# Performance work log

Hardware: AMD Instinct MI355X
Metric: run time of the kernel (lower is better)

Reference implementation:

```python
import jax, jax.numpy as jnp
import numpy as np

N_NODES = 100000
N_EDGES = 1600000
NFEAT = 256
NHID = 128
NCLASS = 2
NEG_SLOPE = 0.2


def setup_inputs() -> dict:
    key = jax.random.key(0)
    ks = jax.random.split(key, 8)
    x = jax.random.normal(ks[0], (N_NODES, NFEAT), dtype=jnp.float32)
    edge_index = jax.random.randint(ks[1], (2, N_EDGES), 0, N_NODES, dtype=jnp.int64)
    # GATConv params (heads=1): lin weight (no bias), att_src, att_dst, bias
    W = jax.random.normal(ks[2], (NFEAT, NHID), dtype=jnp.float32) * (1.0 / np.sqrt(NFEAT))
    att_src = jax.random.normal(ks[3], (NHID,), dtype=jnp.float32) * (1.0 / np.sqrt(NHID))
    att_dst = jax.random.normal(ks[4], (NHID,), dtype=jnp.float32) * (1.0 / np.sqrt(NHID))
    bias_gat = jnp.zeros((NHID,), dtype=jnp.float32)
    fc_w = jax.random.normal(ks[5], (NCLASS, NHID), dtype=jnp.float32) * (1.0 / np.sqrt(NHID))
    fc_b = jnp.zeros((NCLASS,), dtype=jnp.float32)
    return {"x": x, "edge_index": edge_index, "W": W, "att_src": att_src,
            "att_dst": att_dst, "bias_gat": bias_gat, "fc_w": fc_w, "fc_b": fc_b}


def reference(x, edge_index, W, att_src, att_dst, bias_gat, fc_w, fc_b):
    N = x.shape[0]
    # add self loops (PyG GATConv default)
    loops = jnp.broadcast_to(jnp.arange(N, dtype=edge_index.dtype)[None, :], (2, N))
    ei = jnp.concatenate([edge_index, loops], axis=1)  # [2, E+N]
    src, dst = ei[0], ei[1]

    h = x @ W                                 # [N, NHID]
    a_src = h @ att_src                       # [N]
    a_dst = h @ att_dst                       # [N]

    e = jax.nn.leaky_relu(a_src[src] + a_dst[dst], NEG_SLOPE)  # [E+N]
    # segment softmax over destination nodes (every node has a self loop)
    m = jax.ops.segment_max(e, dst, num_segments=N)
    ex = jnp.exp(e - m[dst])
    s = jax.ops.segment_sum(ex, dst, num_segments=N)
    alpha = ex / (s[dst] + 1e-16)             # [E+N]

    msg = h[src] * alpha[:, None]             # [E+N, NHID]
    out = jax.ops.segment_sum(msg, dst, num_segments=N) + bias_gat  # [N, NHID]

    logits = out @ fc_w.T + fc_b              # [N, NCLASS]
    return jax.nn.log_softmax(logits, axis=1)
```

## Files before the change

kernel.cpp:

```cpp
#include <hip/hip_runtime.h>
#include <hip/hip_bf16.h>
#include <stdint.h>

#define N_NODES 100000
#define N_EDGES 1600000
#define NFEAT   256
#define NHID    128
#define NEG_SLOPE 0.2f

#define NB_B       3125
#define SLAB       1024
#define BIN_BLOCKS 512

typedef __attribute__((ext_vector_type(8))) short short8;
typedef __attribute__((ext_vector_type(4))) float f32x4;

__device__ __forceinline__ int clamp_node(int v) {
    unsigned u = (unsigned)v;
    return (u < (unsigned)N_NODES) ? (int)u : 0;
}

__device__ __forceinline__ unsigned short f2bf(float f) {
    unsigned u = __float_as_uint(f);
    return (unsigned short)((u + 0x7fffu + ((u >> 16) & 1u)) >> 16);
}
__device__ __forceinline__ unsigned pkbf(float a, float b) {
    __hip_bfloat162 t = __float22bfloat162_rn(make_float2(a, b));
    return *reinterpret_cast<unsigned*>(&t);
}
__device__ __forceinline__ float bflo(unsigned p) { return __uint_as_float(p << 16); }
__device__ __forceinline__ float bfhi(unsigned p) { return __uint_as_float(p & 0xffff0000u); }

__global__ __launch_bounds__(256) void k_conv(
    const float* __restrict__ W, unsigned short* __restrict__ Wt)
{
    int id = blockIdx.x * 256 + threadIdx.x;
    int n = id >> 8, k = id & 255;
    Wt[id] = f2bf(W[k * NHID + n]);
}

#define LDS_STRIDE 40
__global__ __launch_bounds__(256) void k_gemm_mfma(
    const float* __restrict__ x,
    const unsigned short* __restrict__ Wt,
    const float* __restrict__ atts,
    const float* __restrict__ attd,
    unsigned short* __restrict__ hb,
    float* __restrict__ asrc,
    float* __restrict__ adst)
{
    __shared__ unsigned short As[64 * LDS_STRIDE];
    __shared__ float satt[64][2];

    const int tid  = threadIdx.x;
    const int wave = tid >> 6;
    const int lane = tid & 63;
    const int wm = wave >> 1, wn = wave & 1;
    const int lr = lane & 15, q = lane >> 4;
    const int blockM = blockIdx.x * 64;

    const int ar = tid >> 2;
    const int aq = tid & 3;

    if (tid < 64) { satt[tid][0] = 0.f; satt[tid][1] = 0.f; }

    f32x4 acc[2][4];
#pragma unroll
    for (int a = 0; a < 2; ++a)
#pragma unroll
        for (int b = 0; b < 4; ++b) acc[a][b] = 0.f;

    const int growA = min(blockM + ar, N_NODES - 1);
    const float* xrow = x + (size_t)growA * NFEAT + aq * 8;

    const unsigned short* bbase[4];
#pragma unroll
    for (int nt = 0; nt < 4; ++nt)
        bbase[nt] = Wt + (size_t)(wn * 64 + nt * 16 + lr) * NFEAT + q * 8;

    float4 va0, va1;
    {
        const float4* xp = (const float4*)xrow;
        va0 = xp[0]; va1 = xp[1];
    }
    short8 bcur[4], bnxt[4];
#pragma unroll
    for (int nt = 0; nt < 4; ++nt)
        bcur[nt] = *(const short8*)(bbase[nt]);

#pragma unroll
    for (int kt = 0; kt < 8; ++kt) {
        __syncthreads();
        uint4 pa = make_uint4(pkbf(va0.x, va0.y), pkbf(va0.z, va0.w),
                              pkbf(va1.x, va1.y), pkbf(va1.z, va1.w));
        *(uint4*)&As[ar * LDS_STRIDE + aq * 8] = pa;
        __syncthreads();

        if (kt < 7) {
            const float4* xp = (const float4*)(xrow + (kt + 1) * 32);
            va0 = xp[0]; va1 = xp[1];
#pragma unroll
            for (int nt = 0; nt < 4; ++nt)
                bnxt[nt] = *(const short8*)(bbase[nt] + (kt + 1) * 32);
        }

        short8 af[2];
#pragma unroll
        for (int mt = 0; mt < 2; ++mt)
            af[mt] = *(const short8*)&As[(wm * 32 + mt * 16 + lr) * LDS_STRIDE + q * 8];

#pragma unroll
        for (int mt = 0; mt < 2; ++mt)
#pragma unroll
            for (int nt = 0; nt < 4; ++nt)
                acc[mt][nt] = __builtin_amdgcn_mfma_f32_16x16x32_bf16(
                    af[mt], bcur[nt], acc[mt][nt], 0, 0, 0);

#pragma unroll
        for (int nt = 0; nt < 4; ++nt) bcur[nt] = bnxt[nt];
    }

    float attsv[4], attdv[4];
#pragma unroll
    for (int nt = 0; nt < 4; ++nt) {
        attsv[nt] = atts[wn * 64 + nt * 16 + lr];
        attdv[nt] = attd[wn * 64 + nt * 16 + lr];
    }
#pragma unroll
    for (int mt = 0; mt < 2; ++mt) {
#pragma unroll
        for (int reg = 0; reg < 4; ++reg) {
            float s = 0.f, d = 0.f;
#pragma unroll
            for (int nt = 0; nt < 4; ++nt) {
                float v = acc[mt][nt][reg];
                s += v * attsv[nt];
                d += v * attdv[nt];
            }
#pragma unroll
            for (int mask = 8; mask > 0; mask >>= 1) {
                s += __shfl_xor(s, mask);
                d += __shfl_xor(d, mask);
            }
            if (lr == 0) {
                int lrow = wm * 32 + mt * 16 + q * 4 + reg;
                atomicAdd(&satt[lrow][0], s);
                atomicAdd(&satt[lrow][1], d);
            }
        }
    }

#pragma unroll
    for (int mt = 0; mt < 2; ++mt) {
#pragma unroll
        for (int reg = 0; reg < 4; ++reg) {
            int grow = blockM + wm * 32 + mt * 16 + q * 4 + reg;
            if (grow < N_NODES) {
                unsigned short* hp = hb + (size_t)grow * NHID + wn * 64 + lr;
#pragma unroll
                for (int nt = 0; nt < 4; ++nt)
                    hp[nt * 16] = f2bf(acc[mt][nt][reg]);
            }
        }
    }

    __syncthreads();
    if (tid < 64) {
        int g = blockM + tid;
        if (g < N_NODES) {
            asrc[g] = satt[tid][0];
            adst[g] = satt[tid][1];
        }
    }
}

__global__ __launch_bounds__(256) void k_bin(
    const int* __restrict__ ei, int* __restrict__ gcur,
    unsigned* __restrict__ staged)
{
    __shared__ int hist[NB_B];
    __shared__ int base[NB_B];
    const int t = threadIdx.x;
    const int per = (N_EDGES + BIN_BLOCKS - 1) / BIN_BLOCKS;
    const int e0 = blockIdx.x * per;
    const int e1 = min(e0 + per, N_EDGES);

    for (int i = t; i < NB_B; i += 256) hist[i] = 0;
    __syncthreads();
    for (int e = e0 + t; e < e1; e += 256)
        atomicAdd(&hist[clamp_node(ei[N_EDGES + e]) >> 5], 1);
    __syncthreads();
    for (int i = t; i < NB_B; i += 256) {
        int c = hist[i];
        base[i] = c ? atomicAdd(&gcur[i], c) : 0;
        hist[i] = 0;
    }
    __syncthreads();
    for (int e = e0 + t; e < e1; e += 256) {
        int d = clamp_node(ei[N_EDGES + e]);
        int s = clamp_node(ei[e]);
        int b = d >> 5;
        int pos = base[b] + atomicAdd(&hist[b], 1);
        if (pos < SLAB)
            staged[(size_t)b * SLAB + pos] = (unsigned)s | ((unsigned)(d & 31) << 17);
    }
}

__global__ __launch_bounds__(256) void k_sort_agg(
    const unsigned* __restrict__ staged, const int* __restrict__ gcur,
    const float* __restrict__ asrc, const float* __restrict__ adst,
    const unsigned short* __restrict__ hb,
    const float* __restrict__ bias, const float* __restrict__ fcw,
    const float* __restrict__ fcb, float* __restrict__ out)
{
    __shared__ float2 buf[SLAB];
    __shared__ int hist[32], scanv[32], cntv[32];
    __shared__ float asrc_s[32], adst_s[32];

    const int b = blockIdx.x;
    const int t = threadIdx.x;
    const int eb = b * SLAB;
    const int n = min(gcur[b], SLAB);
    const int nodeStart = b * 32;

    if (t < 32) {
        hist[t] = 0;
        adst_s[t] = adst[nodeStart + t];
        asrc_s[t] = asrc[nodeStart + t];
    }
    __syncthreads();

    for (int j = t; j < n; j += 256)
        atomicAdd(&hist[(staged[eb + j] >> 17) & 31], 1);
    __syncthreads();

    if (t < 32) {
        int v = hist[t];
        int sc = v;
#pragma unroll
        for (int off = 1; off < 32; off <<= 1) {
            int u = __shfl_up(sc, off);
            if (t >= off) sc += u;
        }
        scanv[t] = sc - v;
        cntv[t] = v;
        hist[t] = 0;
    }
    __syncthreads();

    for (int j = t; j < n; j += 256) {
        unsigned pk = staged[eb + j];
        int s  = pk & 0x1FFFF;
        int dl = (pk >> 17) & 31;
        float a = asrc[s] + adst_s[dl];
        a = (a > 0.f) ? a : NEG_SLOPE * a;
        float ew = __expf(fminf(a, 60.f));
        int pos = scanv[dl] + atomicAdd(&hist[dl], 1);
        buf[pos] = make_float2(__int_as_float(s), ew);
    }
    __syncthreads();

    const int wave = t >> 6;
    const int lane = t & 63;
    const unsigned* hrows = (const unsigned*)hb;

    const float b0 = bias[2 * lane], b1 = bias[2 * lane + 1];
    const float w00 = fcw[2 * lane], w01 = fcw[2 * lane + 1];
    const float w10 = fcw[NHID + 2 * lane], w11 = fcw[NHID + 2 * lane + 1];
    const float fb0 = fcb[0], fb1 = fcb[1];

    for (int ln = wave * 8; ln < wave * 8 + 8; ++ln) {
        int i = nodeStart + ln;

        float e0 = asrc_s[ln] + adst_s[ln];
        e0 = (e0 > 0.f) ? e0 : NEG_SLOPE * e0;
        float w = __expf(fminf(e0, 60.f));
        unsigned pself = hrows[(unsigned)i * 64u + lane];
        float accx = w * bflo(pself), accy = w * bfhi(pself), ssum = w;

        const int jb = scanv[ln];
        const int nn = cntv[ln];
        int j = 0;
        for (; j + 8 <= nn; j += 8) {
            float2 m[8];
            unsigned p[8];
#pragma unroll
            for (int u = 0; u < 8; ++u) m[u] = buf[jb + j + u];
#pragma unroll
            for (int u = 0; u < 8; ++u)
                p[u] = hrows[(unsigned)__float_as_int(m[u].x) * 64u + lane];
#pragma unroll
            for (int u = 0; u < 8; ++u) {
                accx += m[u].y * bflo(p[u]);
                accy += m[u].y * bfhi(p[u]);
                ssum += m[u].y;
            }
        }
        for (; j < nn; ++j) {
            float2 m = buf[jb + j];
            unsigned p = hrows[(unsigned)__float_as_int(m.x) * 64u + lane];
            accx += m.y * bflo(p);
            accy += m.y * bfhi(p);
            ssum += m.y;
        }

        float inv = 1.0f / (ssum + 1e-16f);
        float ox = accx * inv + b0;
        float oy = accy * inv + b1;

        float l0 = ox * w00 + oy * w01;
        float l1 = ox * w10 + oy * w11;
#pragma unroll
        for (int off = 32; off > 0; off >>= 1) {
            l0 += __shfl_down(l0, off);
            l1 += __shfl_down(l1, off);
        }
        if (lane == 0) {
            l0 += fb0;
            l1 += fb1;
            float m = fmaxf(l0, l1);
            float ls = m + __logf(__expf(l0 - m) + __expf(l1 - m));
            ((float2*)out)[i] = make_float2(l0 - ls, l1 - ls);
        }
    }
}

extern "C" void kernel_launch(void* const* d_in, const int* in_sizes, int n_in,
                              void* d_out, int out_size, void* d_ws, size_t ws_size,
                              hipStream_t stream)
{
    const float* x    = (const float*)d_in[0];
    const int*   ei   = (const int*)d_in[1];
    const float* W    = (const float*)d_in[2];
    const float* atts = (const float*)d_in[3];
    const float* attd = (const float*)d_in[4];
    const float* bias = (const float*)d_in[5];
    const float* fcw  = (const float*)d_in[6];
    const float* fcb  = (const float*)d_in[7];
    float*       out  = (float*)d_out;

    char* base = (char*)d_ws;
    size_t off = 0;
    auto carve = [&](size_t bytes) -> char* {
        char* p = base + off;
        off = (off + bytes + 255) & ~(size_t)255;
        return p;
    };
    unsigned short* hb     = (unsigned short*)carve((size_t)N_NODES * NHID * 2);
    float*          asrc   = (float*)carve(N_NODES * 4);
    float*          adst   = (float*)carve(N_NODES * 4);
    int*            gcur   = (int*)carve(NB_B * 4);
    unsigned*       staged = (unsigned*)carve((size_t)NB_B * SLAB * 4);
    unsigned short* Wt     = (unsigned short*)carve(NHID * NFEAT * 2);
    (void)ws_size; (void)in_sizes; (void)n_in; (void)out_size;

    hipMemsetAsync(gcur, 0, NB_B * 4, stream);

    const int GB = (N_NODES + 63) / 64;

    k_conv<<<(NHID * NFEAT) / 256, 256, 0, stream>>>(W, Wt);
    k_gemm_mfma<<<GB, 256, 0, stream>>>(x, Wt, atts, attd, hb, asrc, adst);
    k_bin<<<BIN_BLOCKS, 256, 0, stream>>>(ei, gcur, staged);
    k_sort_agg<<<NB_B, 256, 0, stream>>>(staged, gcur, asrc, adst, hb,
                                         bias, fcw, fcb, out);
}
```

Measured before the change: 322.0 us.

## Retile GEMM to 128-row blocks with 1024 threads and W staged in LDS

Result: no change. 318.1 us (-1.2%).

```diff
diff --git a/kernel.cpp b/kernel.cpp
--- a/kernel.cpp
+++ b/kernel.cpp
@@ -40,7 +40,7 @@
 }
 
 #define LDS_STRIDE 40
-__global__ __launch_bounds__(256) void k_gemm_mfma(
+__global__ __launch_bounds__(1024, 8) void k_gemm_mfma(
     const float* __restrict__ x,
     const unsigned short* __restrict__ Wt,
     const float* __restrict__ atts,
@@ -49,75 +49,51 @@
     float* __restrict__ asrc,
     float* __restrict__ adst)
 {
-    __shared__ unsigned short As[64 * LDS_STRIDE];
-    __shared__ float satt[64][2];
+    __shared__ unsigned short As[128 * LDS_STRIDE];
+    __shared__ unsigned short Bs[128 * LDS_STRIDE];
+    __shared__ float satt[128][2];
 
     const int tid  = threadIdx.x;
     const int wave = tid >> 6;
     const int lane = tid & 63;
     const int wm = wave >> 1, wn = wave & 1;
     const int lr = lane & 15, q = lane >> 4;
-    const int blockM = blockIdx.x * 64;
-
-    const int ar = tid >> 2;
-    const int aq = tid & 3;
-
-    if (tid < 64) { satt[tid][0] = 0.f; satt[tid][1] = 0.f; }
-
-    f32x4 acc[2][4];
-#pragma unroll
-    for (int a = 0; a < 2; ++a)
-#pragma unroll
-        for (int b = 0; b < 4; ++b) acc[a][b] = 0.f;
-
-    const int growA = min(blockM + ar, N_NODES - 1);
-    const float* xrow = x + (size_t)growA * NFEAT + aq * 8;
-
-    const unsigned short* bbase[4];
-#pragma unroll
-    for (int nt = 0; nt < 4; ++nt)
-        bbase[nt] = Wt + (size_t)(wn * 64 + nt * 16 + lr) * NFEAT + q * 8;
-
-    float4 va0, va1;
-    {
-        const float4* xp = (const float4*)xrow;
-        va0 = xp[0]; va1 = xp[1];
-    }
-    short8 bcur[4], bnxt[4];
-#pragma unroll
-    for (int nt = 0; nt < 4; ++nt)
-        bcur[nt] = *(const short8*)(bbase[nt]);
-
-#pragma unroll
+    const int blockM = blockIdx.x * 128;
+
+    const int sr = tid >> 3;
+    const int sq = tid & 7;
+
+    if (tid < 128) { satt[tid][0] = 0.f; satt[tid][1] = 0.f; }
+
+    f32x4 acc[4];
+#pragma unroll
+    for (int b = 0; b < 4; ++b) acc[b] = 0.f;
+
+    const int growA = min(blockM + sr, N_NODES - 1);
+    const float* xrow = x + (size_t)growA * NFEAT + sq * 4;
+    const unsigned short* wrow = Wt + sr * NFEAT + sq * 4;
+
+    float4 va = *(const float4*)xrow;
+    uint2  vb = *(const uint2*)wrow;
+
     for (int kt = 0; kt < 8; ++kt) {
         __syncthreads();
-        uint4 pa = make_uint4(pkbf(va0.x, va0.y), pkbf(va0.z, va0.w),
-                              pkbf(va1.x, va1.y), pkbf(va1.z, va1.w));
-        *(uint4*)&As[ar * LDS_STRIDE + aq * 8] = pa;
+        uint2 pa = make_uint2(pkbf(va.x, va.y), pkbf(va.z, va.w));
+        *(uint2*)&As[sr * LDS_STRIDE + sq * 4] = pa;
+        *(uint2*)&Bs[sr * LDS_STRIDE + sq * 4] = vb;
         __syncthreads();
 
         if (kt < 7) {
-            const float4* xp = (const float4*)(xrow + (kt + 1) * 32);
-            va0 = xp[0]; va1 = xp[1];
-#pragma unroll
-            for (int nt = 0; nt < 4; ++nt)
-                bnxt[nt] = *(const short8*)(bbase[nt] + (kt + 1) * 32);
-        }
-
-        short8 af[2];
-#pragma unroll
-        for (int mt = 0; mt < 2; ++mt)
-            af[mt] = *(const short8*)&As[(wm * 32 + mt * 16 + lr) * LDS_STRIDE + q * 8];
-
-#pragma unroll
-        for (int mt = 0; mt < 2; ++mt)
-#pragma unroll
-            for (int nt = 0; nt < 4; ++nt)
-                acc[mt][nt] = __builtin_amdgcn_mfma_f32_16x16x32_bf16(
-                    af[mt], bcur[nt], acc[mt][nt], 0, 0, 0);
-
-#pragma unroll
-        for (int nt = 0; nt < 4; ++nt) bcur[nt] = bnxt[nt];
+            va = *(const float4*)(xrow + (kt + 1) * 32);
+            vb = *(const uint2*)(wrow + (kt + 1) * 32);
+        }
+
+        short8 af = *(const short8*)&As[(wm * 16 + lr) * LDS_STRIDE + q * 8];
+#pragma unroll
+        for (int nt = 0; nt < 4; ++nt) {
+            short8 bfr = *(const short8*)&Bs[(wn * 64 + nt * 16 + lr) * LDS_STRIDE + q * 8];
+            acc[nt] = __builtin_amdgcn_mfma_f32_16x16x32_bf16(af, bfr, acc[nt], 0, 0, 0);
+        }
     }
 
     float attsv[4], attdv[4];
@@ -127,45 +103,39 @@
         attdv[nt] = attd[wn * 64 + nt * 16 + lr];
     }
 #pragma unroll
-    for (int mt = 0; mt < 2; ++mt) {
-#pragma unroll
-        for (int reg = 0; reg < 4; ++reg) {
-            float s = 0.f, d = 0.f;
-#pragma unroll
-            for (int nt = 0; nt < 4; ++nt) {
-                float v = acc[mt][nt][reg];
-                s += v * attsv[nt];
-                d += v * attdv[nt];
-            }
-#pragma unroll
-            for (int mask = 8; mask > 0; mask >>= 1) {
-                s += __shfl_xor(s, mask);
-                d += __shfl_xor(d, mask);
-            }
-            if (lr == 0) {
-                int lrow = wm * 32 + mt * 16 + q * 4 + reg;
-                atomicAdd(&satt[lrow][0], s);
-                atomicAdd(&satt[lrow][1], d);
-            }
-        }
-    }
-
-#pragma unroll
-    for (int mt = 0; mt < 2; ++mt) {
-#pragma unroll
-        for (int reg = 0; reg < 4; ++reg) {
-            int grow = blockM + wm * 32 + mt * 16 + q * 4 + reg;
-            if (grow < N_NODES) {
-                unsigned short* hp = hb + (size_t)grow * NHID + wn * 64 + lr;
-#pragma unroll
-                for (int nt = 0; nt < 4; ++nt)
-                    hp[nt * 16] = f2bf(acc[mt][nt][reg]);
-            }
-        }
-    }
-
-    __syncthreads();
-    if (tid < 64) {
+    for (int reg = 0; reg < 4; ++reg) {
+        float s = 0.f, d = 0.f;
+#pragma unroll
+        for (int nt = 0; nt < 4; ++nt) {
+            float v = acc[nt][reg];
+            s += v * attsv[nt];
+            d += v * attdv[nt];
+        }
+#pragma unroll
+        for (int mask = 8; mask > 0; mask >>= 1) {
+            s += __shfl_xor(s, mask);
+            d += __shfl_xor(d, mask);
+        }
+        if (lr == 0) {
+            int lrow = wm * 16 + q * 4 + reg;
+            atomicAdd(&satt[lrow][0], s);
+            atomicAdd(&satt[lrow][1], d);
+        }
+    }
+
+#pragma unroll
+    for (int reg = 0; reg < 4; ++reg) {
+        int grow = blockM + wm * 16 + q * 4 + reg;
+        if (grow < N_NODES) {
+            unsigned short* hp = hb + (size_t)grow * NHID + wn * 64 + lr;
+#pragma unroll
+            for (int nt = 0; nt < 4; ++nt)
+                hp[nt * 16] = f2bf(acc[nt][reg]);
+        }
+    }
+
+    __syncthreads();
+    if (tid < 128) {
         int g = blockM + tid;
         if (g < N_NODES) {
             asrc[g] = satt[tid][0];
@@ -356,10 +326,10 @@
 
     hipMemsetAsync(gcur, 0, NB_B * 4, stream);
 
-    const int GB = (N_NODES + 63) / 64;
+    const int GB = (N_NODES + 127) / 128;
 
     k_conv<<<(NHID * NFEAT) / 256, 256, 0, stream>>>(W, Wt);
-    k_gemm_mfma<<<GB, 256, 0, stream>>>(x, Wt, atts, attd, hb, asrc, adst);
+    k_gemm_mfma<<<GB, 1024, 0, stream>>>(x, Wt, atts, attd, hb, asrc, adst);
     k_bin<<<BIN_BLOCKS, 256, 0, stream>>>(ei, gcur, staged);
     k_sort_agg<<<NB_B, 256, 0, stream>>>(staged, gcur, asrc, adst, hb,
                                          bias, fcw, fcb, out);
```
